# Kernel optimization log

Measured on AMD Instinct MI355X. Metric: run time of the kernel, lower is better.

The kernel has to match this reference:

```python
import jax, jax.numpy as jnp
import numpy as np

N_NODES = 100000
N_EDGES = 400000
N_GRAPHS = 4000
IN_DIM = 128
HID = 512
N_DESC = 200
N_CLASSES = 2


def setup_inputs() -> dict:
    key = jax.random.key(0)
    ks = jax.random.split(key, 16)
    features = jax.random.normal(ks[0], (N_NODES, IN_DIM), jnp.float32)
    descriptors = jax.random.normal(ks[1], (N_GRAPHS, N_DESC), jnp.float32)
    src = jax.random.randint(ks[2], (N_EDGES,), 0, N_NODES)
    dst = jax.random.randint(ks[3], (N_EDGES,), 0, N_NODES)
    node2graph = jnp.sort(jax.random.randint(ks[4], (N_NODES,), 0, N_GRAPHS))

    def unif(k, shape, fan_out):
        stdv = 1.0 / np.sqrt(fan_out)
        return jax.random.uniform(k, shape, jnp.float32, -stdv, stdv)

    # GCN layer params (torch init: uniform(-1/sqrt(out), 1/sqrt(out)))
    W1 = unif(ks[5], (IN_DIM, HID), HID)
    b1 = unif(ks[6], (HID,), HID)
    W2 = unif(ks[7], (HID, HID), HID)
    b2 = unif(ks[8], (HID,), HID)
    # MLP head (torch Linear default init: uniform(-1/sqrt(fan_in), ...))
    lw1 = unif(ks[9], (HID + N_DESC, 500), HID + N_DESC)
    lb1 = unif(ks[10], (500,), HID + N_DESC)
    lw2 = unif(ks[11], (500, 100), 500)
    lb2 = unif(ks[12], (100,), 500)
    cw = unif(ks[13], (100, N_CLASSES), 100)
    cb = unif(ks[14], (N_CLASSES,), 100)
    return {"features": features, "descriptors": descriptors, "src": src,
            "dst": dst, "node2graph": node2graph, "W1": W1, "b1": b1,
            "W2": W2, "b2": b2, "lw1": lw1, "lb1": lb1, "lw2": lw2,
            "lb2": lb2, "cw": cw, "cb": cb}


def reference(features, descriptors, src, dst, node2graph,
              W1, b1, W2, b2, lw1, lb1, lw2, lb2, cw, cb):
    N = features.shape[0]
    B = descriptors.shape[0]

    def gcn(h, W, b):
        hW = h @ W                                    # [N, F_out]
        # copy_src + sum: gather source features per edge, scatter-sum to dst
        agg = jax.ops.segment_sum(hW[src], dst, num_segments=N)
        return jax.nn.relu(agg + b)

    h = gcn(features, W1, b1)                         # dropout skipped (eval)
    h = gcn(h, W2, b2)

    # dgl.mean_nodes: per-graph mean over nodes
    sums = jax.ops.segment_sum(h, node2graph, num_segments=B)     # [B, HID]
    counts = jax.ops.segment_sum(jnp.ones((N,), h.dtype), node2graph,
                                 num_segments=B)
    hg = sums / jnp.maximum(counts, 1.0)[:, None]

    x = jnp.concatenate([hg, descriptors], axis=1)    # [B, HID+N_DESC]
    x = jax.nn.relu(x @ lw1 + lb1)
    x = jax.nn.relu(x @ lw2 + lb2)
    return x @ cw + cb                                # [B, n_classes]
```

## Files before the change

### kernel.cpp

```cpp
#include <hip/hip_runtime.h>
#include <hip/hip_bf16.h>

#define N_NODES  100000
#define N_EDGES  400000
#define N_GRAPHS 4000
#define IN_DIM   128
#define HID      512
#define N_DESC   200
#define N_CLASSES 2
#define MLP1_OUT 500
#define MLP2_OUT 100
#define XIN_DIM  (HID + N_DESC)
#define XIN_PAD  768

#define SCAN_CHUNK 1024
#define NCHK ((N_NODES + SCAN_CHUNK - 1) / SCAN_CHUNK)

typedef __hip_bfloat16  bf16;
typedef __hip_bfloat162 bf16x2;
typedef short s8v  __attribute__((ext_vector_type(8)));
typedef float f32x4 __attribute__((ext_vector_type(4)));

__device__ __forceinline__ float ldf(const float* p, size_t i) { return p[i]; }
__device__ __forceinline__ float ldf(const bf16* p, size_t i)  { return __bfloat162float(p[i]); }

__device__ __forceinline__ short f2bs(float x) {
    bf16 h = __float2bfloat16(x);
    return __builtin_bit_cast(short, h);
}

__device__ __forceinline__ void gld16(const short* g, short* l) {
    __builtin_amdgcn_global_load_lds(
        (const __attribute__((address_space(1))) unsigned int*)g,
        (__attribute__((address_space(3))) unsigned int*)l, 16, 0, 0);
}

#define MEMFENCE asm volatile("" ::: "memory")

__global__ __launch_bounds__(256)
void detect_dtype_kernel(const unsigned* __restrict__ words, unsigned nw,
                         int* __restrict__ flag)
{
    __shared__ int s_cnt;
    if (threadIdx.x == 0) s_cnt = 0;
    __syncthreads();
    const int SAMPLES = 2048;
    int sane = 0;
    for (int i = threadIdx.x; i < SAMPLES; i += 256) {
        size_t idx = (size_t)(((unsigned long long)i * 2654435761ull) % nw);
        unsigned w = words[idx];
        float f = __uint_as_float((w & 0xFFFFu) << 16);
        float a = fabsf(f);
        if (f == 0.0f || (a > 1e-8f && a < 1e8f)) sane++;
    }
    atomicAdd(&s_cnt, sane);
    __syncthreads();
    if (threadIdx.x == 0) *flag = (s_cnt * 10 > SAMPLES * 6) ? 1 : 0;
}

template<typename FT>
__device__ __forceinline__
void prep_body(int i, const FT* W1, const FT* W2, const FT* lw1, const FT* lw2,
               const FT* b1, const FT* b2, const FT* lb1, const FT* lb2,
               short* W1t, short* W2t, short* lw1t, short* lw2t,
               float* b1f, float* b2f, float* lb1f, float* lb2f)
{
    if (i < 65536) {
        int n = i >> 7, k = i & 127;
        W1t[i] = f2bs(ldf(W1, (size_t)k * HID + n));
        return;
    }
    i -= 65536;
    if (i < 262144) {
        int n = i >> 9, k = i & 511;
        W2t[i] = f2bs(ldf(W2, (size_t)k * HID + n));
        return;
    }
    i -= 262144;
    if (i < 393216) {
        int n = i / XIN_PAD, k = i - n * XIN_PAD;
        lw1t[i] = (n < MLP1_OUT && k < XIN_DIM)
                      ? f2bs(ldf(lw1, (size_t)k * MLP1_OUT + n)) : (short)0;
        return;
    }
    i -= 393216;
    if (i < 65536) {
        int n = i >> 9, k = i & 511;
        lw2t[i] = (n < MLP2_OUT && k < MLP1_OUT)
                      ? f2bs(ldf(lw2, (size_t)k * MLP2_OUT + n)) : (short)0;
        return;
    }
    i -= 65536;
    if (i < 512) { b1f[i] = ldf(b1, i); return; }
    i -= 512;
    if (i < 512) { b2f[i] = ldf(b2, i); return; }
    i -= 512;
    if (i < 512) { lb1f[i] = (i < MLP1_OUT) ? ldf(lb1, i) : 0.f; return; }
    i -= 512;
    if (i < 128) { lb2f[i] = (i < MLP2_OUT) ? ldf(lb2, i) : 0.f; return; }
}

__global__ __launch_bounds__(256)
void prep_weights_kernel(const void* __restrict__ W1, const void* __restrict__ W2,
                         const void* __restrict__ lw1, const void* __restrict__ lw2,
                         const void* __restrict__ b1, const void* __restrict__ b2,
                         const void* __restrict__ lb1, const void* __restrict__ lb2,
                         short* __restrict__ W1t, short* __restrict__ W2t,
                         short* __restrict__ lw1t, short* __restrict__ lw2t,
                         float* __restrict__ b1f, float* __restrict__ b2f,
                         float* __restrict__ lb1f, float* __restrict__ lb2f,
                         const int* __restrict__ flag)
{
    int i = blockIdx.x * 256 + threadIdx.x;
    if (*flag == 0)
        prep_body<float>(i, (const float*)W1, (const float*)W2, (const float*)lw1,
                         (const float*)lw2, (const float*)b1, (const float*)b2,
                         (const float*)lb1, (const float*)lb2,
                         W1t, W2t, lw1t, lw2t, b1f, b2f, lb1f, lb2f);
    else
        prep_body<bf16>(i, (const bf16*)W1, (const bf16*)W2, (const bf16*)lw1,
                        (const bf16*)lw2, (const bf16*)b1, (const bf16*)b2,
                        (const bf16*)lb1, (const bf16*)lb2,
                        W1t, W2t, lw1t, lw2t, b1f, b2f, lb1f, lb2f);
}

__global__ __launch_bounds__(256)
void deg_kernel(const int* __restrict__ dst, int* __restrict__ deg)
{
    int e = blockIdx.x * 256 + threadIdx.x;
    if (e < N_EDGES) atomicAdd(&deg[dst[e]], 1);
}

__global__ __launch_bounds__(256)
void scan_partial_kernel(const int* __restrict__ deg, int* __restrict__ part)
{
    int c = blockIdx.x, t = threadIdx.x;
    int i0 = c * SCAN_CHUNK + t * 4;
    int s = 0;
#pragma unroll
    for (int j = 0; j < 4; j++) {
        int i = i0 + j;
        if (i < N_NODES) s += deg[i];
    }
    __shared__ int red[256];
    red[t] = s;
    __syncthreads();
    for (int off = 128; off > 0; off >>= 1) {
        if (t < off) red[t] += red[t + off];
        __syncthreads();
    }
    if (t == 0) part[c] = red[0];
}

__global__ void scan_parts_kernel(int* __restrict__ part, int* __restrict__ edge_start)
{
    int run = 0;
    for (int c = 0; c < NCHK; c++) { int v = part[c]; part[c] = run; run += v; }
    edge_start[N_NODES] = run;
}

__global__ __launch_bounds__(256)
void scan_final_kernel(const int* __restrict__ deg, const int* __restrict__ part,
                       int* __restrict__ edge_start, int* __restrict__ cursor)
{
    int c = blockIdx.x, t = threadIdx.x;
    int i0 = c * SCAN_CHUNK + t * 4;
    int d[4];
    int tsum = 0;
#pragma unroll
    for (int j = 0; j < 4; j++) {
        int i = i0 + j;
        d[j] = (i < N_NODES) ? deg[i] : 0;
        tsum += d[j];
    }
    __shared__ int s[256];
    s[t] = tsum;
    __syncthreads();
    for (int off = 1; off < 256; off <<= 1) {
        int v = (t >= off) ? s[t - off] : 0;
        __syncthreads();
        s[t] += v;
        __syncthreads();
    }
    int run = part[c] + s[t] - tsum;
#pragma unroll
    for (int j = 0; j < 4; j++) {
        int i = i0 + j;
        if (i < N_NODES) { edge_start[i] = run; cursor[i] = run; run += d[j]; }
    }
}

__global__ __launch_bounds__(256)
void fill_kernel(const int* __restrict__ src, const int* __restrict__ dst,
                 int* __restrict__ cursor, int* __restrict__ csr_src)
{
    int e = blockIdx.x * 256 + threadIdx.x;
    if (e >= N_EDGES) return;
    int p = atomicAdd(&cursor[dst[e]], 1);
    csr_src[p] = src[e];
}

__global__ __launch_bounds__(256)
void gstart_kernel(const int* __restrict__ n2g, int* __restrict__ gstart)
{
    int n = blockIdx.x * 256 + threadIdx.x;
    if (n > N_NODES) return;
    if (n == N_NODES) {
        int last = n2g[N_NODES - 1];
        for (int g = last + 1; g <= N_GRAPHS; g++) gstart[g] = N_NODES;
        return;
    }
    int v = n2g[n];
    int prev = (n == 0) ? -1 : n2g[n - 1];
    for (int g = prev + 1; g <= v; g++) gstart[g] = n;
}

__global__ __launch_bounds__(256)
void gather_feat_kernel(const void* __restrict__ feat_, const int* __restrict__ edge_start,
                        const int* __restrict__ csr_src, bf16* __restrict__ agg1,
                        const int* __restrict__ flag)
{
    int n = blockIdx.x * 4 + (threadIdx.x >> 6);
    if (n >= N_NODES) return;
    int lane = threadIdx.x & 63;
    int e0 = edge_start[n], e1 = edge_start[n + 1];
    float2 acc = {0.f, 0.f};
    if (*flag == 0) {
        const float* feat = (const float*)feat_;
        for (int i = e0; i < e1; i++) {
            int s = csr_src[i];
            float2 f = ((const float2*)(feat + (size_t)s * IN_DIM))[lane];
            acc.x += f.x; acc.y += f.y;
        }
    } else {
        const bf16* feat = (const bf16*)feat_;
        for (int i = e0; i < e1; i++) {
            int s = csr_src[i];
            float2 f = __bfloat1622float2(((const bf16x2*)(feat + (size_t)s * IN_DIM))[lane]);
            acc.x += f.x; acc.y += f.y;
        }
    }
    bf16x2 p;
    p.x = __float2bfloat16(acc.x);
    p.y = __float2bfloat16(acc.y);
    ((bf16x2*)(agg1 + (size_t)n * IN_DIM))[lane] = p;
}

template<int NCT, int ACT>
__global__ __launch_bounds__(256, 4)
void mfma_gemm_kernel(const short* __restrict__ A, const short* __restrict__ Bt,
                      const float* __restrict__ biasf, bf16* __restrict__ Cout,
                      int M, int K, int nrt)
{
    __shared__ short smem[17408];
    short* Cs = smem;

    const int b  = blockIdx.x;
    const int r8 = b & 7;
    const int t0 = b >> 3;
    const int x  = (t0 / NCT) * 8 + r8;
    const int y  = t0 % NCT;
    if (x >= nrt) return;
    const int row0 = x * 128;
    const int col0 = y * 128;

    const int tid  = threadIdx.x;
    const int lane = tid & 63;
    const int w    = tid >> 6;
    const int wr = w >> 1, wc = w & 1;
    const int m  = lane & 15, q = lane >> 4;

    const int rr = lane >> 2;
    const int dc = ((lane & 3) ^ ((lane >> 3) & 3)) * 8;
    const short* pA = A  + (size_t)(row0 + w * 32 + rr) * K + dc;
    const short* pB = Bt + (size_t)(col0 + w * 32 + rr) * K + dc;
    const int cOff = 16 * K;

    const int so = (q ^ ((m >> 1) & 3)) * 8;

    f32x4 acc[4][4];
#pragma unroll
    for (int i = 0; i < 4; i++)
#pragma unroll
        for (int j = 0; j < 4; j++) acc[i][j] = {0.f, 0.f, 0.f, 0.f};

    {
        short* d = smem + w * 1024;
        gld16(pA, d);               gld16(pA + cOff, d + 512);
        gld16(pB, d + 4096);        gld16(pB + cOff, d + 4096 + 512);
        pA += 32; pB += 32;
    }

    const int NT = K >> 5;
    for (int t = 0; t < NT; ++t) {
        const int boff = (t & 1) << 13;
        if (t + 1 < NT) {
            short* d = smem + (8192 - boff) + w * 1024;
            gld16(pA, d);           gld16(pA + cOff, d + 512);
            gld16(pB, d + 4096);    gld16(pB + cOff, d + 4096 + 512);
            pA += 32; pB += 32;
            asm volatile("s_waitcnt vmcnt(4)" ::: "memory");
        } else {
            asm volatile("s_waitcnt vmcnt(0)" ::: "memory");
        }
        __builtin_amdgcn_s_barrier();
        MEMFENCE;

        const short* Ab = smem + boff;
        const short* Bb = smem + boff + 4096;
        s8v av[4], bv[4];
#pragma unroll
        for (int rt = 0; rt < 4; rt++)
            av[rt] = *(const s8v*)&Ab[(wr * 64 + rt * 16 + m) * 32 + so];
#pragma unroll
        for (int ct = 0; ct < 4; ct++)
            bv[ct] = *(const s8v*)&Bb[(wc * 64 + ct * 16 + m) * 32 + so];
#pragma unroll
        for (int rt = 0; rt < 4; rt++)
#pragma unroll
            for (int ct = 0; ct < 4; ct++)
                acc[rt][ct] = __builtin_amdgcn_mfma_f32_16x16x32_bf16(
                    av[rt], bv[ct], acc[rt][ct], 0, 0, 0);

        MEMFENCE;
        __builtin_amdgcn_s_barrier();
        MEMFENCE;
    }

#pragma unroll
    for (int rt = 0; rt < 4; rt++) {
#pragma unroll
        for (int ct = 0; ct < 4; ct++) {
            int lcol = wc * 64 + ct * 16 + m;
            float bv = ACT ? biasf[col0 + lcol] : 0.f;
#pragma unroll
            for (int reg = 0; reg < 4; reg++) {
                int lrow = wr * 64 + rt * 16 + q * 4 + reg;
                float v = acc[rt][ct][reg];
                if constexpr (ACT) {
                    v += bv;
                    v = v > 0.f ? v : 0.f;
                }
                Cs[lrow * 136 + lcol] = f2bs(v);
            }
        }
    }
    __syncthreads();

#pragma unroll
    for (int it = 0; it < 8; it++) {
        int idx = it * 256 + tid;
        int r = idx >> 4;
        int c = (idx & 15) * 8;
        int row = row0 + r;
        if (row < M)
            *(float4*)&Cout[(size_t)row * HID + col0 + c] =
                *(const float4*)&Cs[r * 136 + c];
    }
}

__global__ __launch_bounds__(256)
void gather_pool_kernel(const bf16* __restrict__ G, const int* __restrict__ edge_start,
                        const int* __restrict__ csr_src, const int* __restrict__ gstart,
                        const float* __restrict__ b2f, float* __restrict__ hg)
{
    __shared__ float red[4][HID];
    const int g = blockIdx.x;
    const int tid = threadIdx.x;
    const int lane = tid & 63;
    const int w = tid >> 6;

    float bj[8];
    {
        const float4* bp = (const float4*)(b2f + lane * 8);
        float4 b0 = bp[0], b1 = bp[1];
        bj[0] = b0.x; bj[1] = b0.y; bj[2] = b0.z; bj[3] = b0.w;
        bj[4] = b1.x; bj[5] = b1.y; bj[6] = b1.z; bj[7] = b1.w;
    }

    const int s0 = gstart[g], s1 = gstart[g + 1];
    float hacc[8];
#pragma unroll
    for (int j = 0; j < 8; j++) hacc[j] = 0.f;

    for (int n = s0 + w; n < s1; n += 4) {
        int e0 = edge_start[n], e1 = edge_start[n + 1];
        float racc[8];
#pragma unroll
        for (int j = 0; j < 8; j++) racc[j] = 0.f;
        for (int e = e0; e < e1; ++e) {
            int s = csr_src[e];
            float4 r = ((const float4*)(G + (size_t)s * HID))[lane];
            const bf16x2* p = (const bf16x2*)&r;
#pragma unroll
            for (int qq = 0; qq < 4; qq++) {
                float2 f = __bfloat1622float2(p[qq]);
                racc[2 * qq] += f.x; racc[2 * qq + 1] += f.y;
            }
        }
#pragma unroll
        for (int j = 0; j < 8; j++) {
            float v = racc[j] + bj[j];
            hacc[j] += (v > 0.f ? v : 0.f);
        }
    }

    ((float4*)&red[w][lane * 8])[0] = make_float4(hacc[0], hacc[1], hacc[2], hacc[3]);
    ((float4*)&red[w][lane * 8])[1] = make_float4(hacc[4], hacc[5], hacc[6], hacc[7]);
    __syncthreads();
#pragma unroll
    for (int c = tid; c < HID; c += 256) {
        hg[(size_t)g * HID + c] = red[0][c] + red[1][c] + red[2][c] + red[3][c];
    }
}

__global__ __launch_bounds__(256)
void build_xin_kernel(const float* __restrict__ hg, const int* __restrict__ gstart,
                      const void* __restrict__ desc_, bf16* __restrict__ xinb,
                      const int* __restrict__ flag)
{
    int idx = blockIdx.x * 256 + threadIdx.x;
    if (idx >= N_GRAPHS * XIN_PAD) return;
    int g = idx / XIN_PAD;
    int c = idx - g * XIN_PAD;
    float v;
    if (c < HID) {
        float cnt = (float)(gstart[g + 1] - gstart[g]);
        v = hg[(size_t)g * HID + c] / (cnt > 1.0f ? cnt : 1.0f);
    } else if (c < XIN_DIM) {
        size_t di = (size_t)g * N_DESC + (c - HID);
        v = (*flag == 0) ? ((const float*)desc_)[di]
                         : __bfloat162float(((const bf16*)desc_)[di]);
    } else {
        v = 0.f;
    }
    xinb[idx] = __float2bfloat16(v);
}

__global__ __launch_bounds__(256)
void final_layer_kernel(const bf16* __restrict__ x2b, const void* __restrict__ cw_,
                        const void* __restrict__ cb_, void* __restrict__ out_,
                        const int* __restrict__ flag)
{
    int i = blockIdx.x * 256 + threadIdx.x;
    if (i >= N_GRAPHS * N_CLASSES) return;
    int r = i >> 1, c = i & 1;
    const bf16* x = x2b + (size_t)r * HID;
    if (*flag == 0) {
        const float* cw = (const float*)cw_;
        float acc = ((const float*)cb_)[c];
#pragma unroll 4
        for (int k = 0; k < MLP2_OUT; k++)
            acc += __bfloat162float(x[k]) * cw[k * N_CLASSES + c];
        ((float*)out_)[i] = acc;
    } else {
        const bf16* cw = (const bf16*)cw_;
        float acc = __bfloat162float(((const bf16*)cb_)[c]);
#pragma unroll 4
        for (int k = 0; k < MLP2_OUT; k++)
            acc += __bfloat162float(x[k]) * __bfloat162float(cw[k * N_CLASSES + c]);
        ((bf16*)out_)[i] = __float2bfloat16(acc);
    }
}

static inline size_t align_up(size_t x, size_t a) { return (x + a - 1) & ~(a - 1); }
static inline int swgrid(int nrt, int nct) { return ((nrt + 7) / 8) * 8 * nct; }

extern "C" void kernel_launch(void* const* d_in, const int* in_sizes, int n_in,
                              void* d_out, int out_size, void* d_ws, size_t ws_size,
                              hipStream_t stream)
{
    const void* features    = d_in[0];
    const void* descriptors = d_in[1];
    const int*  src         = (const int*)d_in[2];
    const int*  dst         = (const int*)d_in[3];
    const int*  node2graph  = (const int*)d_in[4];
    const void* W1          = d_in[5];
    const void* b1          = d_in[6];
    const void* W2          = d_in[7];
    const void* b2          = d_in[8];
    const void* lw1         = d_in[9];
    const void* lb1         = d_in[10];
    const void* lw2         = d_in[11];
    const void* lb2         = d_in[12];
    const void* cw          = d_in[13];
    const void* cb          = d_in[14];
    (void)in_sizes; (void)n_in; (void)out_size; (void)ws_size;

    char* ws = (char*)d_ws;
    size_t off = 0;
    bf16* agg1 = (bf16*)(ws + off);
    bf16* G    = (bf16*)(ws + off);
    bf16* xinb = (bf16*)(ws + off);
    bf16* x1b  = (bf16*)(ws + off + (size_t)8 * 1024 * 1024);
    bf16* x2b  = (bf16*)(ws + off + (size_t)16 * 1024 * 1024);
    off = align_up(off + (size_t)N_NODES * HID * sizeof(bf16), 256);
    bf16* h1 = (bf16*)(ws + off);
    off = align_up(off + (size_t)N_NODES * HID * sizeof(bf16), 256);
    float* hg = (float*)(ws + off);
    off = align_up(off + (size_t)N_GRAPHS * HID * sizeof(float), 256);
    int* dflag = (int*)(ws + off);          off = align_up(off + 256, 256);
    int* edge_start = (int*)(ws + off);     off = align_up(off + (N_NODES + 1) * 4, 256);
    int* cursor = (int*)(ws + off);         off = align_up(off + N_NODES * 4, 256);
    int* csr_src = (int*)(ws + off);        off = align_up(off + N_EDGES * 4, 256);
    int* part = (int*)(ws + off);           off = align_up(off + NCHK * 4, 256);
    int* deg = (int*)(ws + off);            off = align_up(off + N_NODES * 4, 256);
    int* gstart = (int*)(ws + off);         off = align_up(off + (N_GRAPHS + 1) * 4, 256);
    short* W1t  = (short*)(ws + off);       off = align_up(off + (size_t)HID * IN_DIM * 2, 256);
    short* W2t  = (short*)(ws + off);       off = align_up(off + (size_t)HID * HID * 2, 256);
    short* lw1t = (short*)(ws + off);       off = align_up(off + (size_t)512 * XIN_PAD * 2, 256);
    short* lw2t = (short*)(ws + off);       off = align_up(off + (size_t)128 * HID * 2, 256);
    float* b1f  = (float*)(ws + off);       off = align_up(off + 512 * 4, 256);
    float* b2f  = (float*)(ws + off);       off = align_up(off + 512 * 4, 256);
    float* lb1f = (float*)(ws + off);       off = align_up(off + 512 * 4, 256);
    float* lb2f = (float*)(ws + off);       off = align_up(off + 128 * 4, 256);

    detect_dtype_kernel<<<1, 256, 0, stream>>>(
        (const unsigned*)features, (unsigned)(N_NODES * IN_DIM / 2), dflag);

    {
        int nblk = (788096 + 255) / 256;
        prep_weights_kernel<<<nblk, 256, 0, stream>>>(
            W1, W2, lw1, lw2, b1, b2, lb1, lb2,
            W1t, W2t, lw1t, lw2t, b1f, b2f, lb1f, lb2f, dflag);
    }

    hipMemsetAsync(deg, 0, N_NODES * 4, stream);
    deg_kernel<<<(N_EDGES + 255) / 256, 256, 0, stream>>>(dst, deg);
    scan_partial_kernel<<<NCHK, 256, 0, stream>>>(deg, part);
    scan_parts_kernel<<<1, 1, 0, stream>>>(part, edge_start);
    scan_final_kernel<<<NCHK, 256, 0, stream>>>(deg, part, edge_start, cursor);
    fill_kernel<<<(N_EDGES + 255) / 256, 256, 0, stream>>>(src, dst, cursor, csr_src);
    gstart_kernel<<<(N_NODES + 256) / 256, 256, 0, stream>>>(node2graph, gstart);

    gather_feat_kernel<<<N_NODES / 4, 256, 0, stream>>>(
        features, edge_start, csr_src, agg1, dflag);
    {
        int nrt = (N_NODES + 127) / 128;
        mfma_gemm_kernel<4, 1><<<swgrid(nrt, 4), 256, 0, stream>>>(
            (const short*)agg1, W1t, b1f, h1, N_NODES, IN_DIM, nrt);
    }

    {
        int nrt = (N_NODES + 127) / 128;
        mfma_gemm_kernel<4, 0><<<swgrid(nrt, 4), 256, 0, stream>>>(
            (const short*)h1, W2t, b2f , G, N_NODES, HID, nrt);
    }
    gather_pool_kernel<<<N_GRAPHS, 256, 0, stream>>>(
        G, edge_start, csr_src, gstart, b2f, hg);

    {
        int nthr = (N_GRAPHS * XIN_PAD + 255) / 256;
        build_xin_kernel<<<nthr, 256, 0, stream>>>(
            hg, gstart, descriptors, xinb, dflag);
    }
    {
        int nrt = (N_GRAPHS + 127) / 128;
        mfma_gemm_kernel<4, 1><<<swgrid(nrt, 4), 256, 0, stream>>>(
            (const short*)xinb, lw1t, lb1f, x1b, N_GRAPHS, XIN_PAD, nrt);
    }
    {
        int nrt = (N_GRAPHS + 127) / 128;
        mfma_gemm_kernel<1, 1><<<swgrid(nrt, 1), 256, 0, stream>>>(
            (const short*)x1b, lw2t, lb2f, x2b, N_GRAPHS, HID, nrt);
    }
    {
        int nthr = (N_GRAPHS * N_CLASSES + 255) / 256;
        final_layer_kernel<<<nthr, 256, 0, stream>>>(
            x2b, cw, cb, d_out, dflag);
    }
}
```

Before: 435.3 us.

## Triple-buffer GEMM K-loop loads and merge gstart into degree kernel

The MFMA GEMM moves from double to triple buffering in LDS, prefetching two K-tiles ahead with adjusted vmcnt waits so global loads have more time to land before they are used. LDS grows from 34 KB to 48 KB per block, which may limit how many blocks fit per CU under launch_bounds(256,4). Separately, the gstart computation is folded into the degree-count kernel as extra blocks, removing one kernel launch.

```diff
diff --git a/kernel.cpp b/kernel.cpp
--- a/kernel.cpp
+++ b/kernel.cpp
@@ -15,6 +15,7 @@
 
 #define SCAN_CHUNK 1024
 #define NCHK ((N_NODES + SCAN_CHUNK - 1) / SCAN_CHUNK)
+#define DEG_BLKS ((N_EDGES + 255) / 256)
 
 typedef __hip_bfloat16  bf16;
 typedef __hip_bfloat162 bf16x2;
@@ -125,10 +126,26 @@
 }
 
 __global__ __launch_bounds__(256)
-void deg_kernel(const int* __restrict__ dst, int* __restrict__ deg)
-{
-    int e = blockIdx.x * 256 + threadIdx.x;
-    if (e < N_EDGES) atomicAdd(&deg[dst[e]], 1);
+void deg_gstart_kernel(const int* __restrict__ dst, int* __restrict__ deg,
+                       const int* __restrict__ n2g, int* __restrict__ gstart)
+{
+    int b = blockIdx.x;
+    int t = threadIdx.x;
+    if (b < DEG_BLKS) {
+        int e = b * 256 + t;
+        if (e < N_EDGES) atomicAdd(&deg[dst[e]], 1);
+        return;
+    }
+    int n = (b - DEG_BLKS) * 256 + t;
+    if (n > N_NODES) return;
+    if (n == N_NODES) {
+        int last = n2g[N_NODES - 1];
+        for (int g = last + 1; g <= N_GRAPHS; g++) gstart[g] = N_NODES;
+        return;
+    }
+    int v = n2g[n];
+    int prev = (n == 0) ? -1 : n2g[n - 1];
+    for (int g = prev + 1; g <= v; g++) gstart[g] = n;
 }
 
 __global__ __launch_bounds__(256)
@@ -198,21 +215,6 @@
     if (e >= N_EDGES) return;
     int p = atomicAdd(&cursor[dst[e]], 1);
     csr_src[p] = src[e];
-}
-
-__global__ __launch_bounds__(256)
-void gstart_kernel(const int* __restrict__ n2g, int* __restrict__ gstart)
-{
-    int n = blockIdx.x * 256 + threadIdx.x;
-    if (n > N_NODES) return;
-    if (n == N_NODES) {
-        int last = n2g[N_NODES - 1];
-        for (int g = last + 1; g <= N_GRAPHS; g++) gstart[g] = N_NODES;
-        return;
-    }
-    int v = n2g[n];
-    int prev = (n == 0) ? -1 : n2g[n - 1];
-    for (int g = prev + 1; g <= v; g++) gstart[g] = n;
 }
 
 __global__ __launch_bounds__(256)
@@ -252,7 +254,7 @@
                       const float* __restrict__ biasf, bf16* __restrict__ Cout,
                       int M, int K, int nrt)
 {
-    __shared__ short smem[17408];
+    __shared__ short smem[24576];
     short* Cs = smem;
 
     const int b  = blockIdx.x;
@@ -289,16 +291,24 @@
         gld16(pA, d);               gld16(pA + cOff, d + 512);
         gld16(pB, d + 4096);        gld16(pB + cOff, d + 4096 + 512);
         pA += 32; pB += 32;
+        d = smem + 8192 + w * 1024;
+        gld16(pA, d);               gld16(pA + cOff, d + 512);
+        gld16(pB, d + 4096);        gld16(pB + cOff, d + 4096 + 512);
+        pA += 32; pB += 32;
     }
 
     const int NT = K >> 5;
+    int bc = 0;
     for (int t = 0; t < NT; ++t) {
-        const int boff = (t & 1) << 13;
-        if (t + 1 < NT) {
-            short* d = smem + (8192 - boff) + w * 1024;
+        if (t + 2 < NT) {
+            int bs2 = bc + 16384;
+            if (bs2 >= 24576) bs2 -= 24576;
+            short* d = smem + bs2 + w * 1024;
             gld16(pA, d);           gld16(pA + cOff, d + 512);
             gld16(pB, d + 4096);    gld16(pB + cOff, d + 4096 + 512);
             pA += 32; pB += 32;
+            asm volatile("s_waitcnt vmcnt(8)" ::: "memory");
+        } else if (t + 2 == NT) {
             asm volatile("s_waitcnt vmcnt(4)" ::: "memory");
         } else {
             asm volatile("s_waitcnt vmcnt(0)" ::: "memory");
@@ -306,8 +316,8 @@
         __builtin_amdgcn_s_barrier();
         MEMFENCE;
 
-        const short* Ab = smem + boff;
-        const short* Bb = smem + boff + 4096;
+        const short* Ab = smem + bc;
+        const short* Bb = smem + bc + 4096;
         s8v av[4], bv[4];
 #pragma unroll
         for (int rt = 0; rt < 4; rt++)
@@ -325,6 +335,7 @@
         MEMFENCE;
         __builtin_amdgcn_s_barrier();
         MEMFENCE;
+        bc = (bc == 16384) ? 0 : bc + 8192;
     }
 
 #pragma unroll
@@ -526,12 +537,15 @@
     }
 
     hipMemsetAsync(deg, 0, N_NODES * 4, stream);
-    deg_kernel<<<(N_EDGES + 255) / 256, 256, 0, stream>>>(dst, deg);
+    {
+        int gblk = (N_NODES + 256) / 256;
+        deg_gstart_kernel<<<DEG_BLKS + gblk, 256, 0, stream>>>(
+            dst, deg, node2graph, gstart);
+    }
     scan_partial_kernel<<<NCHK, 256, 0, stream>>>(deg, part);
     scan_parts_kernel<<<1, 1, 0, stream>>>(part, edge_start);
     scan_final_kernel<<<NCHK, 256, 0, stream>>>(deg, part, edge_start, cursor);
     fill_kernel<<<(N_EDGES + 255) / 256, 256, 0, stream>>>(src, dst, cursor, csr_src);
-    gstart_kernel<<<(N_NODES + 256) / 256, 256, 0, stream>>>(node2graph, gstart);
 
     gather_feat_kernel<<<N_NODES / 4, 256, 0, stream>>>(
         features, edge_start, csr_src, agg1, dflag);
```

New measurement: 425.4 us. -2.3%, faster.
